# Optimization experiments

Measured on AMD Instinct MI355X. Metric: run time of the kernel, lower is better.

## Reference

```python
import jax, jax.numpy as jnp
import numpy as np

# dims: B batch, CIN/COUT channels, K kernel, H/W spatial, S stride, P padding
B, CIN, COUT, K, H, W, S, P = 8, 16, 64, 3, 32, 32, 1, 1
ALPHA, R, N_EKV, VT, VD = 0.05625, 0.1, 1.5, 0.025, 0.1


def setup_inputs() -> dict:
    key = jax.random.key(0)
    k1, k2 = jax.random.split(key)
    x = jax.random.normal(k1, (B, CIN, H, W), dtype=jnp.float32)
    # torch init: uniform_(theta, 1.0, 8.0)
    theta = jax.random.uniform(k2, (COUT, CIN * K * K), dtype=jnp.float32, minval=1.0, maxval=8.0)
    scale = jnp.array(1.0, dtype=jnp.float32)
    return {"x": x, "theta": theta, "scale": scale}


def _unfold(x, k, s, p):
    # torch.nn.Unfold: patches flattened channel-major as (C, kh, kw)
    b, c, h, w = x.shape
    ho = (h + 2 * p - k) // s + 1
    wo = (w + 2 * p - k) // s + 1
    xp = jnp.pad(x, ((0, 0), (0, 0), (p, p), (p, p)))
    patches = jnp.stack(
        [xp[:, :, i:i + ho * s:s, j:j + wo * s:s] for i in range(k) for j in range(k)],
        axis=2,
    )  # (B, C, K*K, Ho, Wo)
    return patches.reshape(b, c * k * k, ho * wo), ho, wo


def _log1p_exp_stable_sq(a):
    # clamp to [-50, 20] then softplus; squared (EKV f)
    a = jnp.clip(a, -50.0, 20.0)
    sp = jnp.log1p(jnp.exp(a))
    return sp * sp


def reference(x, theta, scale):
    theta = jnp.clip(theta, 1.0, 8.0)  # mirrors theta.data.clamp_(1, 8)
    vg, ho, wo = _unfold(x, K, S, P)          # (B, Cin*K^2, L)
    vg = vg[:, None, :, :]                    # (B, 1, Cin*K^2, L)
    vth = theta[None, :, :, None]             # (1, Cout, Cin*K^2, 1)
    denom = 2.0 * N_EKV * VT
    term1 = _log1p_exp_stable_sq((vg - vth) / denom)
    term2 = _log1p_exp_stable_sq((vg - vth - VD) / denom)
    currents = jnp.clip(ALPHA * (term1 - term2), 0.0, None)
    i_k = jnp.sum(currents, axis=2)           # reduce over Cin*K^2 -> (B, Cout, L)
    v_out = i_k * R * scale
    return v_out.reshape(x.shape[0], COUT, ho, wo)
```

## Files before the change

kernel.cpp:

```cpp
#include <hip/hip_runtime.h>
#include <hip/hip_bf16.h>

#define BB 8
#define CIN 16
#define COUT 64
#define HH 32
#define WW 32
#define PH 34
#define PW 34
#define PPLANE (PH * PW)

#define INV_DENOM_LOG2E 19.235933878519388f
#define VD_F 0.1f
#define B_LO (-72.13475204444817f)
#define B_HI (28.85390081777927f)
#define WIN_LO (-0.95f)
#define WIN_HI (1.62f)
#define OUT_CONST (0.4804530139182014f * 0.05625f * 0.1f)

#define EXP2F(x) __builtin_amdgcn_exp2f(x)
#define LOG2F(x) __builtin_amdgcn_logf(x)

__global__ __launch_bounds__(256) void pad_x_kernel(const float* __restrict__ x,
                                                    float* __restrict__ xp) {
    int idx = blockIdx.x * 256 + threadIdx.x;
    int c = idx / PPLANE;
    int r = idx - c * PPLANE;
    int y = r / PW;
    int xc = r - y * PW;
    float v = 0.0f;
    if (y >= 1 && y <= HH && xc >= 1 && xc <= WW) {
        v = x[c * (HH * WW) + (y - 1) * WW + (xc - 1)];
    }
    xp[idx] = v;
}

template <bool PADDED>
__global__ __launch_bounds__(256) void ekv_kernel(const float* __restrict__ xsrc,
                                                  const float* __restrict__ theta,
                                                  const float* __restrict__ scale,
                                                  float* __restrict__ out) {
    int bid = blockIdx.x;
    int co = bid & 63;
    int tile = (bid >> 6) & 3;
    int b = bid >> 8;

    int t = threadIdx.x;
    int ow = t & 31;
    int oh = tile * 8 + (t >> 5);

    __shared__ __align__(16) float s_th[CIN * 12];
    if (t < CIN * 12) {
        int cin = t / 12;
        int j = t - cin * 12;
        float v = 0.0f;
        if (j < 9) {
            float th = theta[co * (CIN * 9) + cin * 9 + j];
            v = fminf(fmaxf(th, 1.0f), 8.0f);
        }
        s_th[t] = v;
    }
    __syncthreads();

    float acc = 0.0f;

    if (PADDED) {
        const float* p = xsrc + (size_t)b * (CIN * PPLANE) + oh * PW + ow;
#pragma unroll 1
        for (int cin = 0; cin < CIN; ++cin, p += PPLANE) {
            float v[9];
#pragma unroll
            for (int dy = 0; dy < 3; ++dy)
#pragma unroll
                for (int dx = 0; dx < 3; ++dx)
                    v[dy * 3 + dx] = p[dy * PW + dx];

            const float* th = s_th + cin * 12;
#pragma unroll
            for (int k = 0; k < 9; ++k) {
                float d = v[k] - th[k];
                if (__any(d > WIN_LO && d < WIN_HI)) {
                    float b1 = fminf(fmaxf(d * INV_DENOM_LOG2E, B_LO), B_HI);
                    float l1 = LOG2F(1.0f + EXP2F(b1));
                    float b2 = fminf(fmaxf((d - VD_F) * INV_DENOM_LOG2E, B_LO), B_HI);
                    float l2 = LOG2F(1.0f + EXP2F(b2));
                    acc += fmaxf(l1 * l1 - l2 * l2, 0.0f);
                }
            }
        }
    } else {
        const float* p = xsrc + (size_t)b * (CIN * HH * WW);
#pragma unroll 1
        for (int cin = 0; cin < CIN; ++cin) {
            float v[9];
#pragma unroll
            for (int dy = 0; dy < 3; ++dy) {
                int y = oh + dy - 1;
#pragma unroll
                for (int dx = 0; dx < 3; ++dx) {
                    int xc = ow + dx - 1;
                    bool ok = ((unsigned)y < HH) && ((unsigned)xc < WW);
                    v[dy * 3 + dx] = ok ? p[cin * (HH * WW) + y * WW + xc] : 0.0f;
                }
            }
            const float* th = s_th + cin * 12;
#pragma unroll
            for (int k = 0; k < 9; ++k) {
                float d = v[k] - th[k];
                if (__any(d > WIN_LO && d < WIN_HI)) {
                    float b1 = fminf(fmaxf(d * INV_DENOM_LOG2E, B_LO), B_HI);
                    float l1 = LOG2F(1.0f + EXP2F(b1));
                    float b2 = fminf(fmaxf((d - VD_F) * INV_DENOM_LOG2E, B_LO), B_HI);
                    float l2 = LOG2F(1.0f + EXP2F(b2));
                    acc += fmaxf(l1 * l1 - l2 * l2, 0.0f);
                }
            }
        }
    }

    float sc = scale[0];
    out[(((size_t)b * COUT + co) * HH + oh) * WW + ow] = acc * (OUT_CONST)*sc;
}

extern "C" void kernel_launch(void* const* d_in, const int* in_sizes, int n_in,
                              void* d_out, int out_size, void* d_ws, size_t ws_size,
                              hipStream_t stream) {
    const float* x = (const float*)d_in[0];
    const float* theta = (const float*)d_in[1];
    const float* scale = (const float*)d_in[2];
    float* out = (float*)d_out;

    constexpr size_t PAD_ELEMS = (size_t)BB * CIN * PPLANE;
    constexpr size_t PAD_BYTES = PAD_ELEMS * sizeof(float);

    if (ws_size >= PAD_BYTES) {
        float* xp = (float*)d_ws;
        pad_x_kernel<<<(int)(PAD_ELEMS / 256), 256, 0, stream>>>(x, xp);
        ekv_kernel<true><<<BB * 4 * COUT, 256, 0, stream>>>(xp, theta, scale, out);
    } else {
        ekv_kernel<false><<<BB * 4 * COUT, 256, 0, stream>>>(x, theta, scale, out);
    }
}
```

Before: 84.22 us.

## Compute two output channels per block and share one exp2 across both softplus terms

Each block now handles two output channels, so every loaded 3x3 input window feeds both and the grid is halved. The second softplus term reuses the first exponential, scaled by exp2(-VD*k), instead of computing its own exp2. The lower clamps and the final max-with-zero are dropped, and the activity window is rewritten as an abs test around its centre. This removes transcendental work and input reloads, at the cost of more registers per thread, a smaller grid, and reliance on the dropped clamps having no effect inside the window.

New measurement: 82.36 us. 1.02x faster.

```diff
diff --git a/kernel.cpp b/kernel.cpp
--- a/kernel.cpp
+++ b/kernel.cpp
@@ -11,11 +11,10 @@
 #define PPLANE (PH * PW)
 
 #define INV_DENOM_LOG2E 19.235933878519388f
-#define VD_F 0.1f
-#define B_LO (-72.13475204444817f)
-#define B_HI (28.85390081777927f)
-#define WIN_LO (-0.95f)
-#define WIN_HI (1.62f)
+#define K2E 0.26359713811472845f
+#define B_HI 28.85390081777927f
+#define WIN_C 0.335f
+#define WIN_HW 1.285f
 #define OUT_CONST (0.4804530139182014f * 0.05625f * 0.1f)
 
 #define EXP2F(x) __builtin_amdgcn_exp2f(x)
@@ -35,34 +34,50 @@
     xp[idx] = v;
 }
 
+__device__ __forceinline__ void ekv_eval(float d, float& acc) {
+    float b1 = d * INV_DENOM_LOG2E;
+    float e1 = EXP2F(b1);
+    float e2 = e1 * K2E;
+    float l1 = fminf(LOG2F(1.0f + e1), B_HI);
+    float l2 = fminf(LOG2F(1.0f + e2), B_HI);
+    acc = fmaf(l1, l1, acc);
+    acc = fmaf(-l2, l2, acc);
+}
+
 template <bool PADDED>
 __global__ __launch_bounds__(256) void ekv_kernel(const float* __restrict__ xsrc,
                                                   const float* __restrict__ theta,
                                                   const float* __restrict__ scale,
                                                   float* __restrict__ out) {
     int bid = blockIdx.x;
-    int co = bid & 63;
-    int tile = (bid >> 6) & 3;
-    int b = bid >> 8;
+    int cog = bid & 31;
+    int tile = (bid >> 5) & 3;
+    int b = bid >> 7;
+    int co0 = cog * 2;
 
     int t = threadIdx.x;
     int ow = t & 31;
     int oh = tile * 8 + (t >> 5);
 
-    __shared__ __align__(16) float s_th[CIN * 12];
-    if (t < CIN * 12) {
-        int cin = t / 12;
-        int j = t - cin * 12;
+    __shared__ __align__(16) float s_th[2 * CIN * 12];
+    if (t < 2 * CIN * 12) {
+    }
+    for (int i = t; i < 2 * CIN * 12; i += 256) {
+        int jj = i / (CIN * 12);
+        int r = i - jj * (CIN * 12);
+        int cin = r / 12;
+        int k = r - cin * 12;
         float v = 0.0f;
-        if (j < 9) {
-            float th = theta[co * (CIN * 9) + cin * 9 + j];
+        if (k < 9) {
+            float th = theta[(co0 + jj) * (CIN * 9) + cin * 9 + k];
             v = fminf(fmaxf(th, 1.0f), 8.0f);
         }
-        s_th[t] = v;
+        s_th[i] = v;
     }
     __syncthreads();
 
-    float acc = 0.0f;
+    float acc0 = 0.0f;
+    float acc1 = 0.0f;
 
     if (PADDED) {
         const float* p = xsrc + (size_t)b * (CIN * PPLANE) + oh * PW + ow;
@@ -75,17 +90,17 @@
                 for (int dx = 0; dx < 3; ++dx)
                     v[dy * 3 + dx] = p[dy * PW + dx];
 
-            const float* th = s_th + cin * 12;
+            const float* th0 = s_th + cin * 12;
+            const float* th1 = s_th + CIN * 12 + cin * 12;
 #pragma unroll
             for (int k = 0; k < 9; ++k) {
-                float d = v[k] - th[k];
-                if (__any(d > WIN_LO && d < WIN_HI)) {
-                    float b1 = fminf(fmaxf(d * INV_DENOM_LOG2E, B_LO), B_HI);
-                    float l1 = LOG2F(1.0f + EXP2F(b1));
-                    float b2 = fminf(fmaxf((d - VD_F) * INV_DENOM_LOG2E, B_LO), B_HI);
-                    float l2 = LOG2F(1.0f + EXP2F(b2));
-                    acc += fmaxf(l1 * l1 - l2 * l2, 0.0f);
-                }
+                float d = v[k] - th0[k];
+                if (__any(fabsf(d - WIN_C) < WIN_HW)) ekv_eval(d, acc0);
+            }
+#pragma unroll
+            for (int k = 0; k < 9; ++k) {
+                float d = v[k] - th1[k];
+                if (__any(fabsf(d - WIN_C) < WIN_HW)) ekv_eval(d, acc1);
             }
         }
     } else {
@@ -103,23 +118,25 @@
                     v[dy * 3 + dx] = ok ? p[cin * (HH * WW) + y * WW + xc] : 0.0f;
                 }
             }
-            const float* th = s_th + cin * 12;
+            const float* th0 = s_th + cin * 12;
+            const float* th1 = s_th + CIN * 12 + cin * 12;
 #pragma unroll
             for (int k = 0; k < 9; ++k) {
-                float d = v[k] - th[k];
-                if (__any(d > WIN_LO && d < WIN_HI)) {
-                    float b1 = fminf(fmaxf(d * INV_DENOM_LOG2E, B_LO), B_HI);
-                    float l1 = LOG2F(1.0f + EXP2F(b1));
-                    float b2 = fminf(fmaxf((d - VD_F) * INV_DENOM_LOG2E, B_LO), B_HI);
-                    float l2 = LOG2F(1.0f + EXP2F(b2));
-                    acc += fmaxf(l1 * l1 - l2 * l2, 0.0f);
-                }
+                float d = v[k] - th0[k];
+                if (__any(fabsf(d - WIN_C) < WIN_HW)) ekv_eval(d, acc0);
+            }
+#pragma unroll
+            for (int k = 0; k < 9; ++k) {
+                float d = v[k] - th1[k];
+                if (__any(fabsf(d - WIN_C) < WIN_HW)) ekv_eval(d, acc1);
             }
         }
     }
 
-    float sc = scale[0];
-    out[(((size_t)b * COUT + co) * HH + oh) * WW + ow] = acc * (OUT_CONST)*sc;
+    float sc = scale[0] * (OUT_CONST);
+    size_t o0 = (((size_t)b * COUT + co0) * HH + oh) * WW + ow;
+    out[o0] = acc0 * sc;
+    out[o0 + (size_t)HH * WW] = acc1 * sc;
 }
 
 extern "C" void kernel_launch(void* const* d_in, const int* in_sizes, int n_in,
@@ -131,13 +148,13 @@
     float* out = (float*)d_out;
 
     constexpr size_t PAD_ELEMS = (size_t)BB * CIN * PPLANE;
-    constexpr size_t PAD_BYTES = PAD_ELEMS * sizeof(float);
+    constexpr size_t PAD_BYTES = (PAD_ELEMS + 4) * sizeof(float);
 
     if (ws_size >= PAD_BYTES) {
         float* xp = (float*)d_ws;
         pad_x_kernel<<<(int)(PAD_ELEMS / 256), 256, 0, stream>>>(x, xp);
-        ekv_kernel<true><<<BB * 4 * COUT, 256, 0, stream>>>(xp, theta, scale, out);
+        ekv_kernel<true><<<BB * 4 * 32, 256, 0, stream>>>(xp, theta, scale, out);
     } else {
-        ekv_kernel<false><<<BB * 4 * COUT, 256, 0, stream>>>(x, theta, scale, out);
+        ekv_kernel<false><<<BB * 4 * 32, 256, 0, stream>>>(x, theta, scale, out);
     }
 }
```

## Share one exp between the two softplus terms and double-buffer channel loads

Applied to the files above, without the earlier changes.

Computes the second softplus term from the first exponential scaled by a constant (exp(-VD/denom)), so each window needs one exp2 instead of two. It also drops the input clamps and the final max-with-zero, and centres the activity window test on a single abs-compare. Channel loads are software-pipelined with two register buffers so the next channel's 9 values load while the current one computes, and launch bounds request higher occupancy. The unpadded fallback is removed, so the workspace is now assumed to be large enough.

New measurement: 75.71 us. 1.11x faster.

```diff
diff --git a/kernel.cpp b/kernel.cpp
--- a/kernel.cpp
+++ b/kernel.cpp
@@ -11,11 +11,10 @@
 #define PPLANE (PH * PW)
 
 #define INV_DENOM_LOG2E 19.235933878519388f
-#define VD_F 0.1f
-#define B_LO (-72.13475204444817f)
-#define B_HI (28.85390081777927f)
-#define WIN_LO (-0.95f)
-#define WIN_HI (1.62f)
+#define K2E 0.26359713811472845f
+#define B_HI 28.85390081777927f
+#define WIN_C 0.46f
+#define WIN_HW 1.16f
 #define OUT_CONST (0.4804530139182014f * 0.05625f * 0.1f)
 
 #define EXP2F(x) __builtin_amdgcn_exp2f(x)
@@ -35,11 +34,40 @@
     xp[idx] = v;
 }
 
-template <bool PADDED>
-__global__ __launch_bounds__(256) void ekv_kernel(const float* __restrict__ xsrc,
-                                                  const float* __restrict__ theta,
-                                                  const float* __restrict__ scale,
-                                                  float* __restrict__ out) {
+__device__ __forceinline__ void ekv_eval(float d, float& acc) {
+    float b1 = d * INV_DENOM_LOG2E;
+    float e1 = EXP2F(b1);
+    float e2 = e1 * K2E;
+    float l1 = fminf(LOG2F(1.0f + e1), B_HI);
+    float l2 = fminf(LOG2F(1.0f + e2), B_HI);
+    acc = fmaf(l1, l1, acc);
+    acc = fmaf(-l2, l2, acc);
+}
+
+__device__ __forceinline__ void load9(const float* __restrict__ p, float* v) {
+#pragma unroll
+    for (int dy = 0; dy < 3; ++dy)
+#pragma unroll
+        for (int dx = 0; dx < 3; ++dx)
+            v[dy * 3 + dx] = p[dy * PW + dx];
+}
+
+__device__ __forceinline__ void compute9(const float* v, const float* __restrict__ sth,
+                                         float& acc) {
+    float th[9];
+#pragma unroll
+    for (int j = 0; j < 9; ++j) th[j] = sth[j];
+#pragma unroll
+    for (int k = 0; k < 9; ++k) {
+        float d = v[k] - th[k];
+        if (__any(fabsf(d - WIN_C) < WIN_HW)) ekv_eval(d, acc);
+    }
+}
+
+__global__ __launch_bounds__(256, 8) void ekv_kernel(const float* __restrict__ xp,
+                                                     const float* __restrict__ theta,
+                                                     const float* __restrict__ scale,
+                                                     float* __restrict__ out) {
     int bid = blockIdx.x;
     int co = bid & 63;
     int tile = (bid >> 6) & 3;
@@ -64,62 +92,20 @@
 
     float acc = 0.0f;
 
-    if (PADDED) {
-        const float* p = xsrc + (size_t)b * (CIN * PPLANE) + oh * PW + ow;
+    const float* p0 = xp + (size_t)b * (CIN * PPLANE) + oh * PW + ow;
+    float va[9], vb[9];
+    load9(p0, va);
 #pragma unroll 1
-        for (int cin = 0; cin < CIN; ++cin, p += PPLANE) {
-            float v[9];
-#pragma unroll
-            for (int dy = 0; dy < 3; ++dy)
-#pragma unroll
-                for (int dx = 0; dx < 3; ++dx)
-                    v[dy * 3 + dx] = p[dy * PW + dx];
-
-            const float* th = s_th + cin * 12;
-#pragma unroll
-            for (int k = 0; k < 9; ++k) {
-                float d = v[k] - th[k];
-                if (__any(d > WIN_LO && d < WIN_HI)) {
-                    float b1 = fminf(fmaxf(d * INV_DENOM_LOG2E, B_LO), B_HI);
-                    float l1 = LOG2F(1.0f + EXP2F(b1));
-                    float b2 = fminf(fmaxf((d - VD_F) * INV_DENOM_LOG2E, B_LO), B_HI);
-                    float l2 = LOG2F(1.0f + EXP2F(b2));
-                    acc += fmaxf(l1 * l1 - l2 * l2, 0.0f);
-                }
-            }
-        }
-    } else {
-        const float* p = xsrc + (size_t)b * (CIN * HH * WW);
-#pragma unroll 1
-        for (int cin = 0; cin < CIN; ++cin) {
-            float v[9];
-#pragma unroll
-            for (int dy = 0; dy < 3; ++dy) {
-                int y = oh + dy - 1;
-#pragma unroll
-                for (int dx = 0; dx < 3; ++dx) {
-                    int xc = ow + dx - 1;
-                    bool ok = ((unsigned)y < HH) && ((unsigned)xc < WW);
-                    v[dy * 3 + dx] = ok ? p[cin * (HH * WW) + y * WW + xc] : 0.0f;
-                }
-            }
-            const float* th = s_th + cin * 12;
-#pragma unroll
-            for (int k = 0; k < 9; ++k) {
-                float d = v[k] - th[k];
-                if (__any(d > WIN_LO && d < WIN_HI)) {
-                    float b1 = fminf(fmaxf(d * INV_DENOM_LOG2E, B_LO), B_HI);
-                    float l1 = LOG2F(1.0f + EXP2F(b1));
-                    float b2 = fminf(fmaxf((d - VD_F) * INV_DENOM_LOG2E, B_LO), B_HI);
-                    float l2 = LOG2F(1.0f + EXP2F(b2));
-                    acc += fmaxf(l1 * l1 - l2 * l2, 0.0f);
-                }
-            }
-        }
+    for (int cin = 0; cin < CIN; cin += 2) {
+        load9(p0 + (cin + 1) * PPLANE, vb);
+        compute9(va, s_th + cin * 12, acc);
+        int nc = cin + 2 < CIN ? cin + 2 : CIN - 1;
+        load9(p0 + nc * PPLANE, va);
+        compute9(vb, s_th + (cin + 1) * 12, acc);
     }
 
-    float sc = scale[0];
-    out[(((size_t)b * COUT + co) * HH + oh) * WW + ow] = acc * (OUT_CONST)*sc;
+    float sc = scale[0] * (OUT_CONST);
+    out[(((size_t)b * COUT + co) * HH + oh) * WW + ow] = acc * sc;
 }
 
 extern "C" void kernel_launch(void* const* d_in, const int* in_sizes, int n_in,
@@ -131,13 +117,11 @@
     float* out = (float*)d_out;
 
     constexpr size_t PAD_ELEMS = (size_t)BB * CIN * PPLANE;
-    constexpr size_t PAD_BYTES = PAD_ELEMS * sizeof(float);
+    constexpr size_t PAD_BYTES = (PAD_ELEMS + 4) * sizeof(float);
 
-    if (ws_size >= PAD_BYTES) {
-        float* xp = (float*)d_ws;
-        pad_x_kernel<<<(int)(PAD_ELEMS / 256), 256, 0, stream>>>(x, xp);
-        ekv_kernel<true><<<BB * 4 * COUT, 256, 0, stream>>>(xp, theta, scale, out);
-    } else {
-        ekv_kernel<false><<<BB * 4 * COUT, 256, 0, stream>>>(x, theta, scale, out);
-    }
+    float* xp = (float*)d_ws;
+    (void)ws_size;
+    pad_x_kernel<<<(int)(PAD_ELEMS / 256), 256, 0, stream>>>(x, xp);
+    ekv_kernel<<<BB * 4 * COUT, 256, 0, stream>>>(xp, theta, scale, out);
+    (void)PAD_BYTES;
 }
```
